# Kernel optimization log

Measured on AMD Instinct MI355X. Metric: run time of the kernel, lower is better.

## Reference

```python
import jax, jax.numpy as jnp
import numpy as np

# ROIAlign config (torchvision semantics, aligned=False)
SPATIAL_SCALE = 0.25
POOLED = 7
SAMPLING_RATIO = 2
MODE = "max"  # from __init__ mode='max'


def setup_inputs() -> dict:
    key = jax.random.key(0)
    kf, kcx, kcy, kw, kh, kb = jax.random.split(key, 6)
    B, C, H, W = 2, 256, 200, 304
    N = 512
    IMG_H, IMG_W = H / SPATIAL_SCALE, W / SPATIAL_SCALE
    feature = jax.random.normal(kf, (B, C, H, W), dtype=jnp.float32)
    cx = jax.random.uniform(kcx, (N,)) * IMG_W
    cy = jax.random.uniform(kcy, (N,)) * IMG_H
    bw = jax.random.uniform(kw, (N,)) * 192.0 + 16.0
    bh = jax.random.uniform(kh, (N,)) * 192.0 + 16.0
    x1 = jnp.clip(cx - bw * 0.5, 0.0, IMG_W - 2.0)
    y1 = jnp.clip(cy - bh * 0.5, 0.0, IMG_H - 2.0)
    x2 = jnp.clip(cx + bw * 0.5, x1 + 1.0, IMG_W - 1.0)
    y2 = jnp.clip(cy + bh * 0.5, y1 + 1.0, IMG_H - 1.0)
    boxes = jnp.stack([x1, y1, x2, y2], axis=1).astype(jnp.float32)
    batch_idx = jax.random.randint(kb, (N,), 0, B, dtype=jnp.int32)
    return {"feature": feature, "boxes": boxes, "batch_idx": batch_idx}


def _sample_coords(start, size):
    # start,size: [N]; returns [N, POOLED*SAMPLING_RATIO] sample coordinates
    bin_sz = size / POOLED                         # [N]
    p = jnp.arange(POOLED, dtype=jnp.float32)      # bin index
    s = (jnp.arange(SAMPLING_RATIO, dtype=jnp.float32) + 0.5) / SAMPLING_RATIO
    # coord = start + (p + s) * bin_sz  -> [N, POOLED, RATIO]
    c = start[:, None, None] + (p[None, :, None] + s[None, None, :]) * bin_sz[:, None, None]
    return c.reshape(c.shape[0], POOLED * SAMPLING_RATIO)


def roi_align(feature, boxes, batch_idx):
    B, C, H, W = feature.shape
    roi = boxes * SPATIAL_SCALE                    # [N,4] in feature coords
    rs_x, rs_y, re_x, re_y = roi[:, 0], roi[:, 1], roi[:, 2], roi[:, 3]
    roi_w = jnp.maximum(re_x - rs_x, 1.0)
    roi_h = jnp.maximum(re_y - rs_y, 1.0)
    ys = _sample_coords(rs_y, roi_h)               # [N, Sy]
    xs = _sample_coords(rs_x, roi_w)               # [N, Sx]
    y = jnp.broadcast_to(ys[:, :, None], (ys.shape[0], ys.shape[1], xs.shape[1]))
    x = jnp.broadcast_to(xs[:, None, :], y.shape)  # [N, Sy, Sx]

    valid = (y > -1.0) & (y < H) & (x > -1.0) & (x < W)
    y = jnp.clip(y, 0.0, H - 1)
    x = jnp.clip(x, 0.0, W - 1)
    y0 = jnp.floor(y).astype(jnp.int32)
    x0 = jnp.floor(x).astype(jnp.int32)
    y1 = jnp.minimum(y0 + 1, H - 1)
    x1 = jnp.minimum(x0 + 1, W - 1)
    ly = y - y0.astype(y.dtype)
    lx = x - x0.astype(x.dtype)
    hy, hx = 1.0 - ly, 1.0 - lx
    b = batch_idx[:, None, None]
    # advanced indexing -> [N, Sy, Sx, C]
    val = (hy * hx)[..., None] * feature[b, :, y0, x0] \
        + (hy * lx)[..., None] * feature[b, :, y0, x1] \
        + (ly * hx)[..., None] * feature[b, :, y1, x0] \
        + (ly * lx)[..., None] * feature[b, :, y1, x1]
    val = jnp.where(valid[..., None], val, 0.0)
    N = boxes.shape[0]
    val = val.reshape(N, POOLED, SAMPLING_RATIO, POOLED, SAMPLING_RATIO, C)
    if MODE == "max":
        out = val.max(axis=(2, 4))                 # [N, PH, PW, C]
    else:
        out = val.mean(axis=(2, 4))
    return jnp.transpose(out, (0, 3, 1, 2))        # [N, C, PH, PW]


def reference(feature, boxes, batch_idx):
    return roi_align(feature, boxes, batch_idx)
```

## Files before the change

kernel.cpp:

```cpp
#include <hip/hip_runtime.h>


#define SPATIAL_SCALE 0.25f
#define POOLED 7
#define SR 2

constexpr int Cc = 256;
constexpr int Hc = 200;
constexpr int Wc = 304;
constexpr int Nc = 512;

constexpr int CG      = 4;
constexpr int TILES   = Cc / CG;
constexpr int NSAMP   = POOLED * SR;
constexpr int NROW    = NSAMP * 2;
constexpr int GRP     = 264;
constexpr int CH_F    = 7 * GRP;
constexpr int BUF_F   = CG * CH_F;
constexpr int CELLS   = POOLED * POOLED;
constexpr int PER_BOX = Cc * CELLS;
constexpr int PLANE   = Hc * Wc;

__global__ __launch_bounds__(64) void box_rank_kernel(
    const float* __restrict__ boxes,
    const int*   __restrict__ batch_idx,
    int*         __restrict__ perm)
{
    const int n = blockIdx.x;
    const int l = threadIdx.x;

    const float cyn  = (boxes[n * 4 + 1] + boxes[n * 4 + 3])
                     * (0.5f * SPATIAL_SCALE);
    const int  bandn = min(3, max(0, (int)(cyn * (4.0f / (float)Hc))));
    const int  keyn  = batch_idx[n] * 4 + bandn;

    int rank = 0;
    #pragma unroll
    for (int m = 0; m < Nc / 64; ++m) {
        const int j = m * 64 + l;
        const float cyj  = (boxes[j * 4 + 1] + boxes[j * 4 + 3])
                         * (0.5f * SPATIAL_SCALE);
        const int  bandj = min(3, max(0, (int)(cyj * (4.0f / (float)Hc))));
        const int  keyj  = batch_idx[j] * 4 + bandj;
        const bool lt = (keyj < keyn) || (keyj == keyn && j < n);
        rank += (int)__popcll(__ballot(lt));
    }
    if (l == 0) perm[rank] = n;
}

template <bool USE_PERM>
__global__ __launch_bounds__(256) void roi_align_max_kernel(
    const float* __restrict__ feature,
    const float* __restrict__ boxes,
    const int*   __restrict__ batch_idx,
    const int*   __restrict__ perm,
    float*       __restrict__ out)
{
    __shared__ float lds[2 * BUF_F];

    const int bid = blockIdx.x;
    const int n = USE_PERM ? perm[(bid & 7) * 64 + (bid >> 3)] : bid;
    const int tid = threadIdx.x;
    const int wv     = tid >> 6;
    const int lane   = tid & 63;
    const int lane16 = lane & 15;
    const int rquad  = lane >> 4;

    const float rsx = boxes[n * 4 + 0] * SPATIAL_SCALE;
    const float rsy = boxes[n * 4 + 1] * SPATIAL_SCALE;
    const float rex = boxes[n * 4 + 2] * SPATIAL_SCALE;
    const float rey = boxes[n * 4 + 3] * SPATIAL_SCALE;
    const float roi_w = fmaxf(rex - rsx, 1.0f);
    const float roi_h = fmaxf(rey - rsy, 1.0f);
    const float bin_w = roi_w / (float)POOLED;
    const float bin_h = roi_h / (float)POOLED;
    const int   b     = batch_idx[n];

    const float x_first = __fadd_rn(rsx, __fmul_rn(0.25f, bin_w));
    const float xc0     = fminf(fmaxf(x_first, 0.0f), (float)(Wc - 1));
    const int   xbase   = ((int)floorf(xc0)) & ~3;

    const float x_last = __fadd_rn(rsx, __fmul_rn(6.75f, bin_w));
    const float xlc    = fminf(fmaxf(x_last, 0.0f), (float)(Wc - 1));
    const int   x0l    = (int)floorf(xlc);
    const int   xlastc = min(x0l + 1, Wc - 1);
    const int   span   = xlastc - xbase + 1;
    const int   nl4    = (span + 4) >> 2;

    int ro[7];
    #pragma unroll
    for (int it = 0; it < 7; ++it) {
        const int  slot  = it * 4 + rquad;
        const int  which = slot >= NSAMP;
        const int  sY    = which ? slot - NSAMP : slot;
        const float py   = fmaf((float)sY, 0.5f, 0.25f);
        const float fy   = __fadd_rn(rsy, __fmul_rn(py, bin_h));
        const float fyc  = fminf(fmaxf(fy, 0.0f), (float)(Hc - 1));
        const int   y0   = (int)floorf(fyc);
        const int   row  = which ? min(y0 + 1, Hc - 1) : y0;
        ro[it] = row * Wc;
    }
    const int  col = min(xbase + lane16 * 4, Wc - 4);
    const bool act = (lane16 < nl4);

    const int cell = min(lane, CELLS - 1);
    const int ph   = cell / POOLED;
    const int pw   = cell - ph * POOLED;

    float w00[2][2], w01[2][2], w10[2][2], w11[2][2];
    int   r0a[2][2], r1a[2][2];
    #pragma unroll
    for (int sy = 0; sy < SR; ++sy) {
        const int   sY  = ph * SR + sy;
        const float py  = (float)ph + ((float)sy + 0.5f) * 0.5f;
        const float fy  = __fadd_rn(rsy, __fmul_rn(py, bin_h));
        const bool  vy  = (fy > -1.0f) && (fy < (float)Hc);
        const float fyc = fminf(fmaxf(fy, 0.0f), (float)(Hc - 1));
        const int   y0i = (int)floorf(fyc);
        const float ly  = fyc - (float)y0i;
        const float hy  = 1.0f - ly;
        #pragma unroll
        for (int sx = 0; sx < SR; ++sx) {
            const float px  = (float)pw + ((float)sx + 0.5f) * 0.5f;
            const float fx  = __fadd_rn(rsx, __fmul_rn(px, bin_w));
            const bool  vx  = (fx > -1.0f) && (fx < (float)Wc);
            const float fxc = fminf(fmaxf(fx, 0.0f), (float)(Wc - 1));
            const int   x0i = (int)floorf(fxc);
            const float lx  = fxc - (float)x0i;
            const float hx  = 1.0f - lx;
            const int   c0  = x0i - xbase;
            const bool  v   = vy && vx;
            w00[sy][sx] = v ? hy * hx : 0.0f;
            w01[sy][sx] = v ? hy * lx : 0.0f;
            w10[sy][sx] = v ? ly * hx : 0.0f;
            w11[sy][sx] = v ? ly * lx : 0.0f;
            const int s0 = sY;
            const int s1 = NSAMP + sY;
            r0a[sy][sx] = (s0 >> 2) * GRP + (s0 & 3) * 64 + c0;
            r1a[sy][sx] = (s1 >> 2) * GRP + (s1 & 3) * 64 + c0;
        }
    }

    const float* __restrict__ gp0 =
        feature + ((size_t)b * Cc + wv) * (size_t)PLANE;

#define ISSUE_TILE(GT, Q)                                                     \
    if (act) {                                                                \
        _Pragma("unroll")                                                     \
        for (int it = 0; it < 7; ++it) {                                      \
            const float* gsrc = (GT) + ro[it] + col;                          \
            const int lofs = __builtin_amdgcn_readfirstlane(                  \
                ((Q) * BUF_F + wv * CH_F + it * GRP) * 4);                    \
            __builtin_amdgcn_global_load_lds(                                 \
                (const __attribute__((address_space(1))) unsigned int*)       \
                    (const void*)gsrc,                                        \
                (__attribute__((address_space(3))) unsigned int*)             \
                    (void*)((char*)lds + lofs),                               \
                16, 0, 0);                                                    \
        }                                                                     \
    }

    ISSUE_TILE(gp0, 0)
    const float* __restrict__ gnext = gp0 + (size_t)CG * PLANE;

    for (int j = 0; j < TILES; ++j) {
        if (j + 1 < TILES) {
            ISSUE_TILE(gnext, ((j + 1) & 1))
            gnext += (size_t)CG * PLANE;
            asm volatile("s_waitcnt vmcnt(7)" ::: "memory");
        } else {
            asm volatile("s_waitcnt vmcnt(0)" ::: "memory");
        }

        const int qb = (j & 1) * BUF_F + wv * CH_F;
        float m = -INFINITY;
        #pragma unroll
        for (int sy = 0; sy < SR; ++sy) {
            #pragma unroll
            for (int sx = 0; sx < SR; ++sx) {
                const int a0 = qb + r0a[sy][sx];
                const int a1 = qb + r1a[sy][sx];
                const float bil = w00[sy][sx] * lds[a0]
                                + w01[sy][sx] * lds[a0 + 1]
                                + w10[sy][sx] * lds[a1]
                                + w11[sy][sx] * lds[a1 + 1];
                m = fmaxf(m, bil);
            }
        }
        if (lane < CELLS)
            out[(size_t)n * PER_BOX + (size_t)(j * CG + wv) * CELLS + cell] = m;
    }
#undef ISSUE_TILE
}

extern "C" void kernel_launch(void* const* d_in, const int* in_sizes, int n_in,
                              void* d_out, int out_size, void* d_ws, size_t ws_size,
                              hipStream_t stream) {
    const float* feature   = (const float*)d_in[0];
    const float* boxes     = (const float*)d_in[1];
    const int*   batch_idx = (const int*)d_in[2];
    float*       out       = (float*)d_out;

    if (d_ws != nullptr && ws_size >= (size_t)Nc * sizeof(int)) {
        int* perm = (int*)d_ws;
        box_rank_kernel<<<Nc, 64, 0, stream>>>(boxes, batch_idx, perm);
        roi_align_max_kernel<true><<<Nc, 256, 0, stream>>>(
            feature, boxes, batch_idx, perm, out);
    } else {
        roi_align_max_kernel<false><<<Nc, 256, 0, stream>>>(
            feature, boxes, batch_idx, nullptr, out);
    }
}
```

Measured before the change: 223.5 us.

## Split each channel's rows across two waves and deepen LDS prefetch to five stages

Doubles the block to 512 threads. Each channel tile is now split between two waves: one loads the upper rows and computes 28 cells, the other loads the lower rows and computes 21 cells. The double-buffered LDS ring becomes a five-deep ring, with four tiles in flight and waits of vmcnt(16) or vmcnt(12) depending on the wave's role. The aim is to hide more global-load latency and spread the bilinear work over more waves, at the cost of more LDS per block and possibly lower occupancy.

```diff
diff --git a/kernel.cpp b/kernel.cpp
--- a/kernel.cpp
+++ b/kernel.cpp
@@ -1,25 +1,28 @@
 #include <hip/hip_runtime.h>
 
 
-#define SPATIAL_SCALE 0.25f
+#define SS 0.25f
 #define POOLED 7
-#define SR 2
 
 constexpr int Cc = 256;
 constexpr int Hc = 200;
 constexpr int Wc = 304;
 constexpr int Nc = 512;
 
-constexpr int CG      = 4;
-constexpr int TILES   = Cc / CG;
-constexpr int NSAMP   = POOLED * SR;
-constexpr int NROW    = NSAMP * 2;
-constexpr int GRP     = 264;
-constexpr int CH_F    = 7 * GRP;
-constexpr int BUF_F   = CG * CH_F;
-constexpr int CELLS   = POOLED * POOLED;
+constexpr int CELLS   = 49;
 constexpr int PER_BOX = Cc * CELLS;
 constexpr int PLANE   = Hc * Wc;
+constexpr int NSAMP   = 14;
+constexpr int TILES   = Cc / 4;
+constexpr int DEPTH   = 5;
+constexpr int GRPF    = 260;
+constexpr int BUF_A   = 4 * GRPF;
+constexpr int BUF_B   = 3 * GRPF;
+constexpr int WAVE_A  = DEPTH * BUF_A;
+constexpr int WAVE_B  = DEPTH * BUF_B;
+constexpr int CH_F    = WAVE_A + WAVE_B;
+constexpr int LDS_F   = 4 * CH_F;
+constexpr size_t WS_NEED = (size_t)Nc * sizeof(int);
 
 __global__ __launch_bounds__(64) void box_rank_kernel(
     const float* __restrict__ boxes,
@@ -29,8 +32,7 @@
     const int n = blockIdx.x;
     const int l = threadIdx.x;
 
-    const float cyn  = (boxes[n * 4 + 1] + boxes[n * 4 + 3])
-                     * (0.5f * SPATIAL_SCALE);
+    const float cyn  = (boxes[n * 4 + 1] + boxes[n * 4 + 3]) * (0.5f * SS);
     const int  bandn = min(3, max(0, (int)(cyn * (4.0f / (float)Hc))));
     const int  keyn  = batch_idx[n] * 4 + bandn;
 
@@ -38,8 +40,7 @@
     #pragma unroll
     for (int m = 0; m < Nc / 64; ++m) {
         const int j = m * 64 + l;
-        const float cyj  = (boxes[j * 4 + 1] + boxes[j * 4 + 3])
-                         * (0.5f * SPATIAL_SCALE);
+        const float cyj  = (boxes[j * 4 + 1] + boxes[j * 4 + 3]) * (0.5f * SS);
         const int  bandj = min(3, max(0, (int)(cyj * (4.0f / (float)Hc))));
         const int  keyj  = batch_idx[j] * 4 + bandj;
         const bool lt = (keyj < keyn) || (keyj == keyn && j < n);
@@ -49,27 +50,35 @@
 }
 
 template <bool USE_PERM>
-__global__ __launch_bounds__(256) void roi_align_max_kernel(
+__global__ __launch_bounds__(512) void roi_align_max_kernel(
     const float* __restrict__ feature,
     const float* __restrict__ boxes,
     const int*   __restrict__ batch_idx,
     const int*   __restrict__ perm,
     float*       __restrict__ out)
 {
-    __shared__ float lds[2 * BUF_F];
+    __shared__ float lds[LDS_F];
 
     const int bid = blockIdx.x;
     const int n = USE_PERM ? perm[(bid & 7) * 64 + (bid >> 3)] : bid;
-    const int tid = threadIdx.x;
-    const int wv     = tid >> 6;
-    const int lane   = tid & 63;
+    const int tid  = threadIdx.x;
+    const int wv   = tid >> 6;
+    const int lane = tid & 63;
+    const int chl  = wv >> 1;
+    const int role = wv & 1;
+    const int NI    = role ? 3 : 4;
+    const int BUF   = role ? BUF_B : BUF_A;
+    const int wbase = chl * CH_F + (role ? WAVE_A : 0);
+    const int HALF  = role ? 6 : 8;
+    const int SYB   = role ? 8 : 0;
+    const int NCELL = role ? 21 : 28;
     const int lane16 = lane & 15;
     const int rquad  = lane >> 4;
 
-    const float rsx = boxes[n * 4 + 0] * SPATIAL_SCALE;
-    const float rsy = boxes[n * 4 + 1] * SPATIAL_SCALE;
-    const float rex = boxes[n * 4 + 2] * SPATIAL_SCALE;
-    const float rey = boxes[n * 4 + 3] * SPATIAL_SCALE;
+    const float rsx = boxes[n * 4 + 0] * SS;
+    const float rsy = boxes[n * 4 + 1] * SS;
+    const float rex = boxes[n * 4 + 2] * SS;
+    const float rey = boxes[n * 4 + 3] * SS;
     const float roi_w = fmaxf(rex - rsx, 1.0f);
     const float roi_h = fmaxf(rey - rsy, 1.0f);
     const float bin_w = roi_w / (float)POOLED;
@@ -87,31 +96,30 @@
     const int   span   = xlastc - xbase + 1;
     const int   nl4    = (span + 4) >> 2;
 
-    int ro[7];
+    int ro[4];
     #pragma unroll
-    for (int it = 0; it < 7; ++it) {
-        const int  slot  = it * 4 + rquad;
-        const int  which = slot >= NSAMP;
-        const int  sY    = which ? slot - NSAMP : slot;
-        const float py   = fmaf((float)sY, 0.5f, 0.25f);
-        const float fy   = __fadd_rn(rsy, __fmul_rn(py, bin_h));
-        const float fyc  = fminf(fmaxf(fy, 0.0f), (float)(Hc - 1));
-        const int   y0   = (int)floorf(fyc);
-        const int   row  = which ? min(y0 + 1, Hc - 1) : y0;
-        ro[it] = row * Wc;
+    for (int i = 0; i < 4; ++i) {
+        const int ls    = i * 4 + rquad;
+        const int which = ls >= HALF;
+        const int sY    = SYB + (which ? ls - HALF : ls);
+        const float py  = fmaf((float)sY, 0.5f, 0.25f);
+        const float fy  = __fadd_rn(rsy, __fmul_rn(py, bin_h));
+        const float fyc = fminf(fmaxf(fy, 0.0f), (float)(Hc - 1));
+        const int   y0  = (int)floorf(fyc);
+        ro[i] = (which ? min(y0 + 1, Hc - 1) : y0) * Wc;
     }
     const int  col = min(xbase + lane16 * 4, Wc - 4);
     const bool act = (lane16 < nl4);
 
-    const int cell = min(lane, CELLS - 1);
-    const int ph   = cell / POOLED;
-    const int pw   = cell - ph * POOLED;
+    const int cidx = min(lane, NCELL - 1);
+    const int ph   = (role ? 4 : 0) + cidx / 7;
+    const int pw   = cidx % 7;
 
     float w00[2][2], w01[2][2], w10[2][2], w11[2][2];
-    int   r0a[2][2], r1a[2][2];
+    int   a0t[2][2], a1t[2][2];
     #pragma unroll
-    for (int sy = 0; sy < SR; ++sy) {
-        const int   sY  = ph * SR + sy;
+    for (int sy = 0; sy < 2; ++sy) {
+        const int   sY  = ph * 2 + sy;
         const float py  = (float)ph + ((float)sy + 0.5f) * 0.5f;
         const float fy  = __fadd_rn(rsy, __fmul_rn(py, bin_h));
         const bool  vy  = (fy > -1.0f) && (fy < (float)Hc);
@@ -120,7 +128,7 @@
         const float ly  = fyc - (float)y0i;
         const float hy  = 1.0f - ly;
         #pragma unroll
-        for (int sx = 0; sx < SR; ++sx) {
+        for (int sx = 0; sx < 2; ++sx) {
             const float px  = (float)pw + ((float)sx + 0.5f) * 0.5f;
             const float fx  = __fadd_rn(rsx, __fmul_rn(px, bin_w));
             const bool  vx  = (fx > -1.0f) && (fx < (float)Wc);
@@ -134,23 +142,20 @@
             w01[sy][sx] = v ? hy * lx : 0.0f;
             w10[sy][sx] = v ? ly * hx : 0.0f;
             w11[sy][sx] = v ? ly * lx : 0.0f;
-            const int s0 = sY;
-            const int s1 = NSAMP + sY;
-            r0a[sy][sx] = (s0 >> 2) * GRP + (s0 & 3) * 64 + c0;
-            r1a[sy][sx] = (s1 >> 2) * GRP + (s1 & 3) * 64 + c0;
-        }
-    }
-
-    const float* __restrict__ gp0 =
-        feature + ((size_t)b * Cc + wv) * (size_t)PLANE;
-
-#define ISSUE_TILE(GT, Q)                                                     \
+            const int lsY = sY - SYB;
+            const int ls0 = lsY;
+            const int ls1 = lsY + HALF;
+            a0t[sy][sx] = (ls0 >> 2) * GRPF + (ls0 & 3) * 64 + c0;
+            a1t[sy][sx] = (ls1 >> 2) * GRPF + (ls1 & 3) * 64 + c0;
+        }
+    }
+
+#define ISSUE(PTR, QOFF)                                                      \
     if (act) {                                                                \
-        _Pragma("unroll")                                                     \
-        for (int it = 0; it < 7; ++it) {                                      \
-            const float* gsrc = (GT) + ro[it] + col;                          \
+        for (int i = 0; i < NI; ++i) {                                        \
+            const float* gsrc = (PTR) + ro[i] + col;                          \
             const int lofs = __builtin_amdgcn_readfirstlane(                  \
-                ((Q) * BUF_F + wv * CH_F + it * GRP) * 4);                    \
+                (wbase + (QOFF) + i * GRPF) * 4);                             \
             __builtin_amdgcn_global_load_lds(                                 \
                 (const __attribute__((address_space(1))) unsigned int*)       \
                     (const void*)gsrc,                                        \
@@ -160,26 +165,41 @@
         }                                                                     \
     }
 
-    ISSUE_TILE(gp0, 0)
-    const float* __restrict__ gnext = gp0 + (size_t)CG * PLANE;
-
-    for (int j = 0; j < TILES; ++j) {
-        if (j + 1 < TILES) {
-            ISSUE_TILE(gnext, ((j + 1) & 1))
-            gnext += (size_t)CG * PLANE;
-            asm volatile("s_waitcnt vmcnt(7)" ::: "memory");
+    const float* gp0 = feature + ((size_t)b * Cc + chl) * (size_t)PLANE;
+    {
+        const float* gpt = gp0;
+        #pragma unroll
+        for (int tt = 0; tt < 4; ++tt) {
+            ISSUE(gpt, tt * BUF)
+            gpt += (size_t)4 * PLANE;
+        }
+    }
+    const float* gIss = gp0 + (size_t)16 * PLANE;
+    int qI = 4 * BUF;
+    int qC = 0;
+    const int QMAX = DEPTH * BUF;
+    float* outp = out + (size_t)n * PER_BOX + chl * CELLS
+                + (role ? 28 : 0) + cidx;
+
+    for (int t = 0; t < TILES; ++t) {
+        if (t < TILES - 4) {
+            ISSUE(gIss, qI)
+            gIss += (size_t)4 * PLANE;
+            qI += BUF; if (qI == QMAX) qI = 0;
+            if (role == 0) asm volatile("s_waitcnt vmcnt(16)" ::: "memory");
+            else           asm volatile("s_waitcnt vmcnt(12)" ::: "memory");
         } else {
             asm volatile("s_waitcnt vmcnt(0)" ::: "memory");
         }
 
-        const int qb = (j & 1) * BUF_F + wv * CH_F;
+        const int qb = wbase + qC;
         float m = -INFINITY;
         #pragma unroll
-        for (int sy = 0; sy < SR; ++sy) {
+        for (int sy = 0; sy < 2; ++sy) {
             #pragma unroll
-            for (int sx = 0; sx < SR; ++sx) {
-                const int a0 = qb + r0a[sy][sx];
-                const int a1 = qb + r1a[sy][sx];
+            for (int sx = 0; sx < 2; ++sx) {
+                const int a0 = qb + a0t[sy][sx];
+                const int a1 = qb + a1t[sy][sx];
                 const float bil = w00[sy][sx] * lds[a0]
                                 + w01[sy][sx] * lds[a0 + 1]
                                 + w10[sy][sx] * lds[a1]
@@ -187,10 +207,11 @@
                 m = fmaxf(m, bil);
             }
         }
-        if (lane < CELLS)
-            out[(size_t)n * PER_BOX + (size_t)(j * CG + wv) * CELLS + cell] = m;
-    }
-#undef ISSUE_TILE
+        if (lane < NCELL) *outp = m;
+        outp += 4 * CELLS;
+        qC += BUF; if (qC == QMAX) qC = 0;
+    }
+#undef ISSUE
 }
 
 extern "C" void kernel_launch(void* const* d_in, const int* in_sizes, int n_in,
@@ -201,13 +222,13 @@
     const int*   batch_idx = (const int*)d_in[2];
     float*       out       = (float*)d_out;
 
-    if (d_ws != nullptr && ws_size >= (size_t)Nc * sizeof(int)) {
+    if (d_ws != nullptr && ws_size >= WS_NEED) {
         int* perm = (int*)d_ws;
         box_rank_kernel<<<Nc, 64, 0, stream>>>(boxes, batch_idx, perm);
-        roi_align_max_kernel<true><<<Nc, 256, 0, stream>>>(
+        roi_align_max_kernel<true><<<Nc, 512, 0, stream>>>(
             feature, boxes, batch_idx, perm, out);
     } else {
-        roi_align_max_kernel<false><<<Nc, 256, 0, stream>>>(
+        roi_align_max_kernel<false><<<Nc, 512, 0, stream>>>(
             feature, boxes, batch_idx, nullptr, out);
     }
 }
```

Result: slower. 246.8 us (+10.4%).
